# Kernel tuning notes

Measured on AMD Instinct MI355X. Metric: run time of the kernel, lower is better.

## Reference

```python
import jax, jax.numpy as jnp
import numpy as np

B, S, D, H = 4, 2048, 1024, 16
DH = D // H


def setup_inputs() -> dict:
    key = jax.random.key(0)
    ks = jax.random.split(key, 5)
    std = 1.0 / np.sqrt(D)
    return {
        "x": jax.random.normal(ks[0], (B, S, D), dtype=jnp.float32),
        "mask": jnp.ones((S, S), dtype=bool),  # unused by the original forward
        "Wq": jax.random.normal(ks[1], (D, D), dtype=jnp.float32) * std,
        "Wk": jax.random.normal(ks[2], (D, D), dtype=jnp.float32) * std,
        "Wv": jax.random.normal(ks[3], (D, D), dtype=jnp.float32) * std,
        "Wout": jax.random.normal(ks[4], (D, D), dtype=jnp.float32) * std,
    }


def reference(x, mask, Wq, Wk, Wv, Wout):
    n, s, d = x.shape
    scale = 1.0 / np.sqrt(DH).astype(np.float32)
    q = (x @ Wq).reshape(n, s, H, DH)
    k = (x @ Wk).reshape(n, s, H, DH)
    v = (x @ Wv).reshape(n, s, H, DH)
    # scores [n, q, k, h]; softmax over k axis (dim=-2 in original)
    attn = jnp.einsum('nqhd,nkhd->nqkh', q, k) * scale
    attn = jax.nn.softmax(attn, axis=-2)
    z = jnp.einsum('nqkh,nkhd->nqhd', attn, v).reshape(n, s, d)
    z = jnp.einsum('nqd,de->nqe', z, Wout)
    return x + z
```

## Files before the change

### kernel.cpp

```cpp
#include <hip/hip_runtime.h>

#define Bn 4
#define Sn 2048
#define Dn 1024
#define Hn 16
#define DHn 64

typedef float f32x4 __attribute__((ext_vector_type(4)));
typedef short bf16x8 __attribute__((ext_vector_type(8)));
typedef unsigned short u16;
typedef unsigned int u32;
typedef unsigned short u16x8 __attribute__((ext_vector_type(8)));
typedef unsigned short u16x4 __attribute__((ext_vector_type(4)));
typedef u32 u32x4 __attribute__((ext_vector_type(4)));

union B8 { u32x4 u; bf16x8 s; };

__device__ __forceinline__ u16 f2bf(float f){
  union { float f; u32 u; } v; v.f = f;
  return (u16)((v.u + 0x7fffu + ((v.u >> 16) & 1u)) >> 16);
}

__device__ __forceinline__ u32 pack_bf2(float lo, float hi){
  union { float f; u32 u; } a, b;
  a.f = lo; b.f = hi;
  return __builtin_amdgcn_perm(b.u + 0x8000u, a.u + 0x8000u, 0x07060302u);
}

#if __has_builtin(__builtin_amdgcn_exp2f)
#define EXP2(x) __builtin_amdgcn_exp2f(x)
#define QSCALE 0.18033688011112042f
#else
#define EXP2(x) __expf(x)
#define QSCALE 0.125f
#endif

#if __has_builtin(__builtin_amdgcn_global_load_lds)
#define G2L16(l, g) __builtin_amdgcn_global_load_lds((const __attribute__((address_space(1))) u32*)(g), \
                                                     (__attribute__((address_space(3))) u32*)(l), 16, 0, 0)
#else
#define G2L16(l, g) (*(bf16x8*)(l) = *(const bf16x8*)(g))
#endif

__global__ void cast_x_kernel(const float* __restrict__ x, u16* __restrict__ xb){
  size_t i = ((size_t)blockIdx.x * 256 + threadIdx.x) * 8;
  float4 f0 = *(const float4*)(x + i);
  float4 f1 = *(const float4*)(x + i + 4);
  u16x8 o;
  o[0]=f2bf(f0.x); o[1]=f2bf(f0.y); o[2]=f2bf(f0.z); o[3]=f2bf(f0.w);
  o[4]=f2bf(f1.x); o[5]=f2bf(f1.y); o[6]=f2bf(f1.z); o[7]=f2bf(f1.w);
  *(u16x8*)(xb + i) = o;
}

__global__ void cast_w_kernel(const float* __restrict__ Wq, const float* __restrict__ Wk,
                              const float* __restrict__ Wv, const float* __restrict__ Wo,
                              u16* __restrict__ wt_all){
  __shared__ u16 tile[64*66];
  const int t = threadIdx.x;
  const int k0 = blockIdx.x * 64, n0 = blockIdx.y * 64, z = blockIdx.z;
  const float* w = (z == 0) ? Wq : (z == 1) ? Wk : (z == 2) ? Wv : Wo;
  const float scale = (z == 0) ? QSCALE : 1.0f;
  u16* wt = wt_all + (size_t)z * Dn * Dn;
  #pragma unroll
  for (int i = 0; i < 4; i++){
    int idx = i*256 + t;
    int r = idx >> 4, c4 = (idx & 15) * 4;
    float4 f = *(const float4*)(w + (size_t)(k0 + r)*Dn + n0 + c4);
    tile[r*66 + c4 + 0] = f2bf(f.x * scale);
    tile[r*66 + c4 + 1] = f2bf(f.y * scale);
    tile[r*66 + c4 + 2] = f2bf(f.z * scale);
    tile[r*66 + c4 + 3] = f2bf(f.w * scale);
  }
  __syncthreads();
  #pragma unroll
  for (int i = 0; i < 4; i++){
    int idx = i*256 + t;
    int nr = idx >> 4, kc4 = (idx & 15) * 4;
    u16x4 o;
    o[0] = tile[(kc4+0)*66 + nr];
    o[1] = tile[(kc4+1)*66 + nr];
    o[2] = tile[(kc4+2)*66 + nr];
    o[3] = tile[(kc4+3)*66 + nr];
    *(u16x4*)(wt + (size_t)(n0 + nr)*Dn + k0 + kc4) = o;
  }
}

__launch_bounds__(256)
__global__ void gemm_qkv_kernel(const u16* __restrict__ xb, const u16* __restrict__ wt_all,
                                u16* __restrict__ qb, u16* __restrict__ kb, u16* __restrict__ vtb){
  __shared__ u16 As[128*32];
  __shared__ u16 Bs[128*32];
  __shared__ u16 Cs[128*136];
  const int t = threadIdx.x;
  const int wave = t >> 6, lane = t & 63;
  const int ln = lane & 15, quad = lane >> 4;
  const int wm = wave >> 1, wn = wave & 1;
  const int n0 = blockIdx.x * 128;
  const int m0 = blockIdx.y * 128;
  const int zsel = blockIdx.z;
  const u16* wt = wt_all + (size_t)zsel * Dn * Dn;

  f32x4 acc[4][4] = {};

  for (int kt = 0; kt < Dn; kt += 32){
    __syncthreads();
    #pragma unroll
    for (int i = 0; i < 2; i++){
      int idx = i*256 + t;
      int r = idx >> 2, c8 = (idx & 3) * 8;
      G2L16(&As[idx*8], xb + (size_t)(m0 + r)*Dn + kt + c8);
      G2L16(&Bs[idx*8], wt + (size_t)(n0 + r)*Dn + kt + c8);
    }
    __syncthreads();
    bf16x8 a[4], b[4];
    #pragma unroll
    for (int rb = 0; rb < 4; rb++) a[rb] = *(const bf16x8*)&As[(wm*64 + rb*16 + ln)*32 + quad*8];
    #pragma unroll
    for (int cb = 0; cb < 4; cb++) b[cb] = *(const bf16x8*)&Bs[(wn*64 + cb*16 + ln)*32 + quad*8];
    #pragma unroll
    for (int rb = 0; rb < 4; rb++)
      #pragma unroll
      for (int cb = 0; cb < 4; cb++)
        acc[rb][cb] = __builtin_amdgcn_mfma_f32_16x16x32_bf16(a[rb], b[cb], acc[rb][cb], 0, 0, 0);
  }

  if (zsel < 2){
    #pragma unroll
    for (int rb = 0; rb < 4; rb++)
      #pragma unroll
      for (int cb = 0; cb < 4; cb++)
        #pragma unroll
        for (int reg = 0; reg < 4; reg++)
          Cs[(wm*64 + rb*16 + quad*4 + reg)*136 + wn*64 + cb*16 + ln] = f2bf(acc[rb][cb][reg]);
  } else {
    #pragma unroll
    for (int rb = 0; rb < 4; rb++)
      #pragma unroll
      for (int cb = 0; cb < 4; cb++){
        u16x4 o;
        #pragma unroll
        for (int reg = 0; reg < 4; reg++) o[reg] = f2bf(acc[rb][cb][reg]);
        *(u16x4*)&Cs[(wn*64 + cb*16 + ln)*136 + wm*64 + rb*16 + quad*4] = o;
      }
  }
  __syncthreads();

  if (zsel < 2){
    u16* outp = (zsel == 0) ? qb : kb;
    #pragma unroll
    for (int i = 0; i < 8; i++){
      int idx = i*256 + t;
      int r = idx >> 4, c8 = (idx & 15) * 8;
      bf16x8 vdat = *(const bf16x8*)&Cs[r*136 + c8];
      int row = m0 + r, bb = row >> 11, s = row & 2047;
      int col = n0 + c8, hh = col >> 6, d = col & 63;
      *(bf16x8*)(outp + (((size_t)bb*Hn + hh)*Sn + s)*DHn + d) = vdat;
    }
  } else {
    #pragma unroll
    for (int i = 0; i < 8; i++){
      int idx = i*256 + t;
      int c = idx >> 4, r8 = (idx & 15) * 8;
      bf16x8 vdat = *(const bf16x8*)&Cs[c*136 + r8];
      int col = n0 + c, hh = col >> 6, d = col & 63;
      int row = m0 + r8, bb = row >> 11, s = row & 2047;
      *(bf16x8*)(vtb + (((size_t)bb*Hn + hh)*DHn + d)*Sn + s) = vdat;
    }
  }
}

__launch_bounds__(256, 2)
__global__ void attn_kernel(const u16* q, const u16* __restrict__ k,
                            const u16* __restrict__ vt, u16* z){
  __shared__ u16 Ks[64*72];
  __shared__ u16 Vs[64*72];
  const int t = threadIdx.x;
  const int wave = t >> 6, lane = t & 63;
  const int ln = lane & 15, quad = lane >> 4;
  const int qt = blockIdx.x, h = blockIdx.y, b = blockIdx.z;
  const size_t bh = (size_t)b * Hn + h;
  const int q0 = qt*256 + wave*64;
  const u16* qp = q + bh * Sn * DHn;
  const u16* kp = k + bh * Sn * DHn;
  const u16* vp = vt + bh * DHn * Sn;

  bf16x8 qf[4][2];
  #pragma unroll
  for (int n = 0; n < 4; n++)
    #pragma unroll
    for (int kq = 0; kq < 2; kq++)
      qf[n][kq] = *(const bf16x8*)(qp + (size_t)(q0 + n*16 + ln)*DHn + kq*32 + quad*8);

  f32x4 zacc[4][4] = {};
  float dacc[4] = {0.f, 0.f, 0.f, 0.f};

  for (int kt = 0; kt < Sn/64; kt++){
    __syncthreads();
    #pragma unroll
    for (int i = 0; i < 2; i++){
      int idx = i*256 + t;
      int r = idx >> 3, c8 = (idx & 7) * 8;
      *(bf16x8*)&Ks[r*72 + c8] = *(const bf16x8*)(kp + (size_t)(kt*64 + r)*DHn + c8);
      *(bf16x8*)&Vs[r*72 + c8] = *(const bf16x8*)(vp + (size_t)r*Sn + kt*64 + c8);
    }
    __syncthreads();

    f32x4 sacc[4][4] = {};
    #pragma unroll
    for (int kq = 0; kq < 2; kq++){
      bf16x8 ka[4];
      #pragma unroll
      for (int mt = 0; mt < 4; mt++)
        ka[mt] = *(const bf16x8*)&Ks[(mt*16 + ln)*72 + kq*32 + quad*8];
      #pragma unroll
      for (int mt = 0; mt < 4; mt++)
        #pragma unroll
        for (int n = 0; n < 4; n++)
          sacc[mt][n] = __builtin_amdgcn_mfma_f32_16x16x32_bf16(ka[mt], qf[n][kq], sacc[mt][n], 0, 0, 0);
    }

    u32 pk[4][4][2];
    #pragma unroll
    for (int mt = 0; mt < 4; mt++)
      #pragma unroll
      for (int n = 0; n < 4; n++){
        f32x4 s = sacc[mt][n];
        float e0 = EXP2(s[0]), e1 = EXP2(s[1]), e2 = EXP2(s[2]), e3 = EXP2(s[3]);
        dacc[n] += (e0 + e1) + (e2 + e3);
        pk[mt][n][0] = pack_bf2(e0, e1);
        pk[mt][n][1] = pack_bf2(e2, e3);
      }

    #pragma unroll
    for (int ks = 0; ks < 2; ks++){
      B8 pb[4];
      #pragma unroll
      for (int n = 0; n < 4; n++)
        pb[n].u = (u32x4){pk[2*ks][n][0], pk[2*ks][n][1], pk[2*ks+1][n][0], pk[2*ks+1][n][1]};
      #pragma unroll
      for (int mtd = 0; mtd < 4; mtd++){
        const u16* vr = &Vs[(mtd*16 + ln)*72 + ks*32 + quad*4];
        uint2 v0 = *(const uint2*)vr;
        uint2 v1 = *(const uint2*)(vr + 16);
        B8 va; va.u = (u32x4){v0.x, v0.y, v1.x, v1.y};
        #pragma unroll
        for (int n = 0; n < 4; n++)
          zacc[mtd][n] = __builtin_amdgcn_mfma_f32_16x16x32_bf16(va.s, pb[n].s, zacc[mtd][n], 0, 0, 0);
      }
    }
  }

  float inv[4];
  #pragma unroll
  for (int n = 0; n < 4; n++){
    float d = dacc[n];
    d += __shfl_xor(d, 16, 64);
    d += __shfl_xor(d, 32, 64);
    inv[n] = 1.0f / d;
  }

  #pragma unroll
  for (int mtd = 0; mtd < 4; mtd++)
    #pragma unroll
    for (int n = 0; n < 4; n++){
      u16x4 o;
      #pragma unroll
      for (int j = 0; j < 4; j++) o[j] = f2bf(zacc[mtd][n][j] * inv[n]);
      *(u16x4*)(z + (bh*Sn + (size_t)(q0 + n*16 + ln))*DHn + mtd*16 + quad*4) = o;
    }
}

__launch_bounds__(256)
__global__ void gemm_out_kernel(const u16* __restrict__ zb, const u16* __restrict__ wt,
                                const float* __restrict__ x, float* __restrict__ out){
  __shared__ u16 As[128*32];
  __shared__ u16 Bs[128*32];
  const int t = threadIdx.x;
  const int wave = t >> 6, lane = t & 63;
  const int ln = lane & 15, quad = lane >> 4;
  const int wm = wave >> 1, wn = wave & 1;
  const int n0 = blockIdx.x * 128;
  const int m0 = blockIdx.y * 128;

  f32x4 acc[4][4] = {};

  for (int kt = 0; kt < Dn; kt += 32){
    int h = kt >> 6, d0 = kt & 63;
    __syncthreads();
    #pragma unroll
    for (int i = 0; i < 2; i++){
      int idx = i*256 + t;
      int r = idx >> 2, c8 = (idx & 3) * 8;
      int row = m0 + r;
      int bb = row >> 11, s = row & 2047;
      G2L16(&As[idx*8], zb + (((size_t)bb*Hn + h)*Sn + s)*DHn + d0 + c8);
      G2L16(&Bs[idx*8], wt + (size_t)(n0 + r)*Dn + kt + c8);
    }
    __syncthreads();
    bf16x8 a[4], b[4];
    #pragma unroll
    for (int rb = 0; rb < 4; rb++) a[rb] = *(const bf16x8*)&As[(wm*64 + rb*16 + ln)*32 + quad*8];
    #pragma unroll
    for (int cb = 0; cb < 4; cb++) b[cb] = *(const bf16x8*)&Bs[(wn*64 + cb*16 + ln)*32 + quad*8];
    #pragma unroll
    for (int rb = 0; rb < 4; rb++)
      #pragma unroll
      for (int cb = 0; cb < 4; cb++)
        acc[rb][cb] = __builtin_amdgcn_mfma_f32_16x16x32_bf16(a[rb], b[cb], acc[rb][cb], 0, 0, 0);
  }

  #pragma unroll
  for (int rb = 0; rb < 4; rb++)
    #pragma unroll
    for (int cb = 0; cb < 4; cb++)
      #pragma unroll
      for (int reg = 0; reg < 4; reg++){
        int row = m0 + wm*64 + rb*16 + quad*4 + reg;
        int col = n0 + wn*64 + cb*16 + ln;
        size_t off = (size_t)row*Dn + col;
        out[off] = acc[rb][cb][reg] + x[off];
      }
}

extern "C" void kernel_launch(void* const* d_in, const int* in_sizes, int n_in,
                              void* d_out, int out_size, void* d_ws, size_t ws_size,
                              hipStream_t stream){
  const float* x    = (const float*)d_in[0];
  const float* Wq   = (const float*)d_in[2];
  const float* Wk   = (const float*)d_in[3];
  const float* Wv   = (const float*)d_in[4];
  const float* Wout = (const float*)d_in[5];
  float* out = (float*)d_out;

  u16* ws = (u16*)d_ws;
  const size_t NW = (size_t)Dn * Dn;
  const size_t NX = (size_t)Bn * Sn * Dn;
  u16* wt  = ws;
  u16* xb  = wt + 4*NW;
  u16* qb  = xb + NX;
  u16* kb  = qb + NX;
  u16* vtb = kb + NX;

  dim3 blk(256);
  cast_x_kernel   <<<dim3((unsigned)(NX/(256*8))), blk, 0, stream>>>(x, xb);
  cast_w_kernel   <<<dim3(16,16,4), blk, 0, stream>>>(Wq, Wk, Wv, Wout, wt);
  gemm_qkv_kernel <<<dim3(8,64,3), blk, 0, stream>>>(xb, wt, qb, kb, vtb);
  attn_kernel     <<<dim3(8,16,4), blk, 0, stream>>>(qb, kb, vtb, qb);
  gemm_out_kernel <<<dim3(8,64), blk, 0, stream>>>(qb, wt + 3*NW, x, out);
}
```

Before: 297.1 us.

## Double-buffer K/V tiles in attention, permute V layout, fuse cast kernels

```diff
diff --git a/kernel.cpp b/kernel.cpp
--- a/kernel.cpp
+++ b/kernel.cpp
@@ -14,7 +14,7 @@
 typedef unsigned short u16x4 __attribute__((ext_vector_type(4)));
 typedef u32 u32x4 __attribute__((ext_vector_type(4)));
 
-union B8 { u32x4 u; bf16x8 s; };
+union B8 { u32x4 u; bf16x8 s; u16x8 h; };
 
 __device__ __forceinline__ u16 f2bf(float f){
   union { float f; u32 u; } v; v.f = f;
@@ -24,7 +24,7 @@
 __device__ __forceinline__ u32 pack_bf2(float lo, float hi){
   union { float f; u32 u; } a, b;
   a.f = lo; b.f = hi;
-  return __builtin_amdgcn_perm(b.u + 0x8000u, a.u + 0x8000u, 0x07060302u);
+  return __builtin_amdgcn_perm(b.u, a.u, 0x07060302u);
 }
 
 #if __has_builtin(__builtin_amdgcn_exp2f)
@@ -42,22 +42,25 @@
 #define G2L16(l, g) (*(bf16x8*)(l) = *(const bf16x8*)(g))
 #endif
 
-__global__ void cast_x_kernel(const float* __restrict__ x, u16* __restrict__ xb){
-  size_t i = ((size_t)blockIdx.x * 256 + threadIdx.x) * 8;
-  float4 f0 = *(const float4*)(x + i);
-  float4 f1 = *(const float4*)(x + i + 4);
-  u16x8 o;
-  o[0]=f2bf(f0.x); o[1]=f2bf(f0.y); o[2]=f2bf(f0.z); o[3]=f2bf(f0.w);
-  o[4]=f2bf(f1.x); o[5]=f2bf(f1.y); o[6]=f2bf(f1.z); o[7]=f2bf(f1.w);
-  *(u16x8*)(xb + i) = o;
-}
-
-__global__ void cast_w_kernel(const float* __restrict__ Wq, const float* __restrict__ Wk,
-                              const float* __restrict__ Wv, const float* __restrict__ Wo,
-                              u16* __restrict__ wt_all){
+__global__ void prep_kernel(const float* __restrict__ x,
+                            const float* __restrict__ Wq, const float* __restrict__ Wk,
+                            const float* __restrict__ Wv, const float* __restrict__ Wo,
+                            u16* __restrict__ xb, u16* __restrict__ wt_all){
   __shared__ u16 tile[64*66];
   const int t = threadIdx.x;
-  const int k0 = blockIdx.x * 64, n0 = blockIdx.y * 64, z = blockIdx.z;
+  if (blockIdx.x < 4096){
+    size_t i = ((size_t)blockIdx.x * 256 + t) * 8;
+    float4 f0 = *(const float4*)(x + i);
+    float4 f1 = *(const float4*)(x + i + 4);
+    u16x8 o;
+    o[0]=f2bf(f0.x); o[1]=f2bf(f0.y); o[2]=f2bf(f0.z); o[3]=f2bf(f0.w);
+    o[4]=f2bf(f1.x); o[5]=f2bf(f1.y); o[6]=f2bf(f1.z); o[7]=f2bf(f1.w);
+    *(u16x8*)(xb + i) = o;
+    return;
+  }
+  const int wi = blockIdx.x - 4096;
+  const int z = wi >> 8, r8 = wi & 255;
+  const int k0 = (r8 >> 4) * 64, n0 = (r8 & 15) * 64;
   const float* w = (z == 0) ? Wq : (z == 1) ? Wk : (z == 2) ? Wv : Wo;
   const float scale = (z == 0) ? QSCALE : 1.0f;
   u16* wt = wt_all + (size_t)z * Dn * Dn;
@@ -172,8 +175,8 @@
 __launch_bounds__(256, 2)
 __global__ void attn_kernel(const u16* q, const u16* __restrict__ k,
                             const u16* __restrict__ vt, u16* z){
-  __shared__ u16 Ks[64*72];
-  __shared__ u16 Vs[64*72];
+  __shared__ u16 Ks[2][64*72];
+  __shared__ u16 Vs[2][64*72];
   const int t = threadIdx.x;
   const int wave = t >> 6, lane = t & 63;
   const int ln = lane & 15, quad = lane >> 4;
@@ -194,16 +197,39 @@
   f32x4 zacc[4][4] = {};
   float dacc[4] = {0.f, 0.f, 0.f, 0.f};
 
+  bf16x8 rk[2], rv[2];
+
+  #pragma unroll
+  for (int i = 0; i < 2; i++){
+    int idx = i*256 + t, r = idx >> 3, a = idx & 7;
+    rk[i] = *(const bf16x8*)(kp + (size_t)r*DHn + a*8);
+    rv[i] = *(const bf16x8*)(vp + (size_t)r*Sn + a*8);
+  }
+  #pragma unroll
+  for (int i = 0; i < 2; i++){
+    int idx = i*256 + t, r = idx >> 3, a = idx & 7;
+    *(bf16x8*)&Ks[0][r*72 + a*8] = rk[i];
+    int ksg = a >> 2, q1 = ((a&3)*2)&3, h1 = (a&3) >> 1;
+    u16x4 lo = *(u16x4*)&rv[i];
+    u16x4 hi = *((u16x4*)&rv[i] + 1);
+    *(u16x4*)&Vs[0][r*72 + ksg*32 + q1*8 + h1*4] = lo;
+    *(u16x4*)&Vs[0][r*72 + ksg*32 + ((q1+1)&3)*8 + h1*4] = hi;
+  }
+
   for (int kt = 0; kt < Sn/64; kt++){
-    __syncthreads();
-    #pragma unroll
-    for (int i = 0; i < 2; i++){
-      int idx = i*256 + t;
-      int r = idx >> 3, c8 = (idx & 7) * 8;
-      *(bf16x8*)&Ks[r*72 + c8] = *(const bf16x8*)(kp + (size_t)(kt*64 + r)*DHn + c8);
-      *(bf16x8*)&Vs[r*72 + c8] = *(const bf16x8*)(vp + (size_t)r*Sn + kt*64 + c8);
-    }
-    __syncthreads();
+    const int cur = kt & 1;
+    __syncthreads();
+
+    if (kt + 1 < Sn/64){
+      #pragma unroll
+      for (int i = 0; i < 2; i++){
+        int idx = i*256 + t, r = idx >> 3, a = idx & 7;
+        rk[i] = *(const bf16x8*)(kp + (size_t)((kt+1)*64 + r)*DHn + a*8);
+        rv[i] = *(const bf16x8*)(vp + (size_t)r*Sn + (kt+1)*64 + a*8);
+      }
+    }
+    const u16* Kc = Ks[cur];
+    const u16* Vc = Vs[cur];
 
     f32x4 sacc[4][4] = {};
     #pragma unroll
@@ -211,7 +237,7 @@
       bf16x8 ka[4];
       #pragma unroll
       for (int mt = 0; mt < 4; mt++)
-        ka[mt] = *(const bf16x8*)&Ks[(mt*16 + ln)*72 + kq*32 + quad*8];
+        ka[mt] = *(const bf16x8*)&Kc[(mt*16 + ln)*72 + kq*32 + quad*8];
       #pragma unroll
       for (int mt = 0; mt < 4; mt++)
         #pragma unroll
@@ -219,33 +245,37 @@
           sacc[mt][n] = __builtin_amdgcn_mfma_f32_16x16x32_bf16(ka[mt], qf[n][kq], sacc[mt][n], 0, 0, 0);
     }
 
-    u32 pk[4][4][2];
-    #pragma unroll
-    for (int mt = 0; mt < 4; mt++)
-      #pragma unroll
-      for (int n = 0; n < 4; n++){
-        f32x4 s = sacc[mt][n];
-        float e0 = EXP2(s[0]), e1 = EXP2(s[1]), e2 = EXP2(s[2]), e3 = EXP2(s[3]);
-        dacc[n] += (e0 + e1) + (e2 + e3);
-        pk[mt][n][0] = pack_bf2(e0, e1);
-        pk[mt][n][1] = pack_bf2(e2, e3);
-      }
-
     #pragma unroll
     for (int ks = 0; ks < 2; ks++){
       B8 pb[4];
       #pragma unroll
-      for (int n = 0; n < 4; n++)
-        pb[n].u = (u32x4){pk[2*ks][n][0], pk[2*ks][n][1], pk[2*ks+1][n][0], pk[2*ks+1][n][1]};
+      for (int n = 0; n < 4; n++){
+        f32x4 s0 = sacc[2*ks][n], s1 = sacc[2*ks+1][n];
+        float a0 = EXP2(s0[0]), a1 = EXP2(s0[1]), a2 = EXP2(s0[2]), a3 = EXP2(s0[3]);
+        float b0 = EXP2(s1[0]), b1 = EXP2(s1[1]), b2 = EXP2(s1[2]), b3 = EXP2(s1[3]);
+        dacc[n] += ((a0 + a1) + (a2 + a3)) + ((b0 + b1) + (b2 + b3));
+        pb[n].u = (u32x4){pack_bf2(a0, a1), pack_bf2(a2, a3), pack_bf2(b0, b1), pack_bf2(b2, b3)};
+      }
       #pragma unroll
       for (int mtd = 0; mtd < 4; mtd++){
-        const u16* vr = &Vs[(mtd*16 + ln)*72 + ks*32 + quad*4];
-        uint2 v0 = *(const uint2*)vr;
-        uint2 v1 = *(const uint2*)(vr + 16);
-        B8 va; va.u = (u32x4){v0.x, v0.y, v1.x, v1.y};
+        bf16x8 va = *(const bf16x8*)&Vc[(mtd*16 + ln)*72 + ks*32 + quad*8];
         #pragma unroll
         for (int n = 0; n < 4; n++)
-          zacc[mtd][n] = __builtin_amdgcn_mfma_f32_16x16x32_bf16(va.s, pb[n].s, zacc[mtd][n], 0, 0, 0);
+          zacc[mtd][n] = __builtin_amdgcn_mfma_f32_16x16x32_bf16(va, pb[n].s, zacc[mtd][n], 0, 0, 0);
+      }
+    }
+
+    if (kt + 1 < Sn/64){
+      const int nxt = (kt+1) & 1;
+      #pragma unroll
+      for (int i = 0; i < 2; i++){
+        int idx = i*256 + t, r = idx >> 3, a = idx & 7;
+        *(bf16x8*)&Ks[nxt][r*72 + a*8] = rk[i];
+        int ksg = a >> 2, q1 = ((a&3)*2)&3, h1 = (a&3) >> 1;
+        u16x4 lo = *(u16x4*)&rv[i];
+        u16x4 hi = *((u16x4*)&rv[i] + 1);
+        *(u16x4*)&Vs[nxt][r*72 + ksg*32 + q1*8 + h1*4] = lo;
+        *(u16x4*)&Vs[nxt][r*72 + ksg*32 + ((q1+1)&3)*8 + h1*4] = hi;
       }
     }
   }
@@ -342,8 +372,7 @@
   u16* vtb = kb + NX;
 
   dim3 blk(256);
-  cast_x_kernel   <<<dim3((unsigned)(NX/(256*8))), blk, 0, stream>>>(x, xb);
-  cast_w_kernel   <<<dim3(16,16,4), blk, 0, stream>>>(Wq, Wk, Wv, Wout, wt);
+  prep_kernel     <<<dim3(4096 + 1024), blk, 0, stream>>>(x, Wq, Wk, Wv, Wout, xb, wt);
   gemm_qkv_kernel <<<dim3(8,64,3), blk, 0, stream>>>(xb, wt, qb, kb, vtb);
   attn_kernel     <<<dim3(8,16,4), blk, 0, stream>>>(qb, kb, vtb, qb);
   gemm_out_kernel <<<dim3(8,64), blk, 0, stream>>>(qb, wt + 3*NW, x, out);
```

After: 289.4 us. 2.6% less time.
